# Kernel optimization log

Hardware: AMD Instinct MI355X
Metric: run time of the kernel (lower is better)

Reference implementation:

```python
import jax, jax.numpy as jnp
import numpy as np

DIM = 512; H = 8; KH = 2; G = 4; DH = 64        # dim, q heads, kv heads, GQA group, head dim
BALL = 128; SEL = 64; TOPK = 2; PDIM = 3        # sliding ball, compress/selection block, topk, pos dim
SCALE = DH ** -0.5


def _rms_norm(x, gamma):
    return x * jax.lax.rsqrt(jnp.mean(x * x, axis=-1, keepdims=True) + 1e-6) * gamma


def _rotary(t):
    # t: (B, h, S, DH); GPT-NeoX style rotate-half rotary embedding
    S = t.shape[-2]
    inv = 1.0 / (10000.0 ** (jnp.arange(0, DH, 2, dtype=jnp.float32) / DH))
    f = jnp.arange(S, dtype=jnp.float32)[:, None] * inv          # (S, DH/2)
    cos = jnp.concatenate([jnp.cos(f), jnp.cos(f)], -1)
    sin = jnp.concatenate([jnp.sin(f), jnp.sin(f)], -1)
    t1, t2 = jnp.split(t, 2, -1)
    return t * cos + jnp.concatenate([-t2, t1], -1) * sin


def _forward(x, pos, pe_w, pe_b, gamma, wq, wk, wv, k_pos, v_pos,
             k_w1, k_b1, k_w2, k_b2, v_w1, v_b1, v_w2, v_b2,
             mem_k, mem_v, w_combine, w_out, num_batches):
    B = num_batches
    # relative position of leaves wrt ball center (no-grad in original)
    p = jax.lax.stop_gradient(pos).reshape(-1, SEL, PDIM)
    rel = (p - p.mean(axis=1, keepdims=True)).reshape(-1, PDIM)
    x = x + rel @ pe_w + pe_b
    x = x.reshape(B, -1, DIM)
    S = x.shape[1]
    nb = S // SEL
    h = _rms_norm(x, gamma)
    q = (h @ wq).reshape(B, S, H, DH).transpose(0, 2, 1, 3)      # (B,H,S,DH)
    k = (h @ wk).reshape(B, S, KH, DH).transpose(0, 2, 1, 3)     # (B,KH,S,DH)
    v = (h @ wv).reshape(B, S, KH, DH).transpose(0, 2, 1, 3)
    qr, kr = _rotary(q), _rotary(k)

    # --- compressed branch: per-block intra-pos emb + MLP compression ---
    kb = k.reshape(B, KH, nb, SEL, DH) + k_pos[None, :, None]
    vb = v.reshape(B, KH, nb, SEL, DH) + v_pos[None, :, None]
    ck = jax.nn.relu(kb.reshape(B, KH, nb, SEL * DH) @ k_w1 + k_b1) @ k_w2 + k_b2
    cv = jax.nn.relu(vb.reshape(B, KH, nb, SEL * DH) @ v_w1 + v_b1) @ v_w2 + v_b2
    ck = jnp.concatenate([jnp.broadcast_to(mem_k[None], (B, KH, 1, DH)), ck], axis=2)
    cv = jnp.concatenate([jnp.broadcast_to(mem_v[None], (B, KH, 1, DH)), cv], axis=2)
    qg = qr.reshape(B, KH, G, S, DH)
    csim = jnp.einsum('bkgsd,bknd->bkgsn', qg, ck) * SCALE
    cattn = jax.nn.softmax(csim, axis=-1)
    cout = jnp.einsum('bkgsn,bknd->bkgsd', cattn, cv).reshape(B, H, S, DH)

    # --- top-k block selection from compressed attention importance ---
    imp = cattn[..., 1:].mean(axis=2)                            # share over grouped q heads: (B,KH,S,nb)
    imp_blk = imp.reshape(B, KH, nb, SEL, nb).mean(axis=3)       # per query block: (B,KH,nb,nb)
    _, sel = jax.lax.top_k(imp_blk, TOPK)                        # (B,KH,nb,TOPK)

    # --- fine branch: each query block attends own + TOPK selected blocks ---
    kblk = kr.reshape(B, KH, nb, SEL, DH)
    vblk = v.reshape(B, KH, nb, SEL, DH)
    gather = jax.vmap(jax.vmap(lambda t, s: t[s]))               # (nb,SEL,DH),(nb,TOPK)->(nb,TOPK,SEL,DH)
    fk = jnp.concatenate([gather(kblk, sel), kblk[:, :, :, None]], axis=3)
    fv = jnp.concatenate([gather(vblk, sel), vblk[:, :, :, None]], axis=3)
    fk = fk.reshape(B, KH, nb, (TOPK + 1) * SEL, DH)
    fv = fv.reshape(B, KH, nb, (TOPK + 1) * SEL, DH)
    qb = qr.reshape(B, KH, G, nb, SEL, DH)
    fsim = jnp.einsum('bkgnqd,bknmd->bkgnqm', qb, fk) * SCALE
    fout = jnp.einsum('bkgnqm,bknmd->bkgnqd', jax.nn.softmax(fsim, -1), fv)
    fout = fout.reshape(B, H, S, DH)

    # --- sliding branch: MiniBallAttn = plain SDPA within balls of size 128 ---
    nw = S // BALL
    qw = qr.reshape(B, H, nw, BALL, DH)
    kw = jnp.repeat(kr, G, axis=1).reshape(B, H, nw, BALL, DH)
    vw = jnp.repeat(v, G, axis=1).reshape(B, H, nw, BALL, DH)
    ssim = jnp.einsum('bhnqd,bhnkd->bhnqk', qw, kw) * SCALE
    sout = jnp.einsum('bhnqk,bhnkd->bhnqd', jax.nn.softmax(ssim, -1), vw)
    sout = sout.reshape(B, H, S, DH)

    # --- sigmoid-gated strategy combine, merge heads, out projection ---
    gates = jax.nn.sigmoid(h @ w_combine).reshape(B, S, H, 3).transpose(0, 2, 1, 3)
    out = gates[..., 0:1] * cout + gates[..., 1:2] * fout + gates[..., 2:3] * sout
    out = out.transpose(0, 2, 1, 3).reshape(B, S, H * DH) @ w_out
    return out.reshape(-1, DIM)


def setup_inputs() -> dict:
    key = jax.random.key(0)
    ks = jax.random.split(key, 16)
    Bn, S = 8, 4096
    N = Bn * S
    CD = SEL * DH
    def lin(k, fi, fo):
        return (jax.random.normal(k, (fi, fo), jnp.float32) / np.sqrt(fi)).astype(jnp.float32)
    return {
        'x': jax.random.normal(ks[0], (N, DIM), jnp.float32),
        'pos': jax.random.normal(ks[1], (N, PDIM), jnp.float32),
        'pe_w': lin(ks[2], PDIM, DIM),
        'pe_b': jnp.zeros((DIM,), jnp.float32),
        'gamma': jnp.ones((DIM,), jnp.float32),
        'wq': lin(ks[3], DIM, H * DH),
        'wk': lin(ks[4], DIM, KH * DH),
        'wv': lin(ks[5], DIM, KH * DH),
        'k_pos': jax.random.normal(ks[6], (KH, SEL, DH), jnp.float32) * 0.02,
        'v_pos': jax.random.normal(ks[7], (KH, SEL, DH), jnp.float32) * 0.02,
        'k_w1': lin(ks[8], CD, CD), 'k_b1': jnp.zeros((CD,), jnp.float32),
        'k_w2': lin(ks[9], CD, DH), 'k_b2': jnp.zeros((DH,), jnp.float32),
        'v_w1': lin(ks[10], CD, CD), 'v_b1': jnp.zeros((CD,), jnp.float32),
        'v_w2': lin(ks[11], CD, DH), 'v_b2': jnp.zeros((DH,), jnp.float32),
        'mem_k': jax.random.normal(ks[12], (KH, 1, DH), jnp.float32) * 0.02,
        'mem_v': jax.random.normal(ks[13], (KH, 1, DH), jnp.float32) * 0.02,
        'w_combine': lin(ks[14], DIM, 3 * H),
        'w_out': lin(ks[15], H * DH, DIM),
        'num_batches': 8,
    }


def reference(x, pos, pe_w, pe_b, gamma, wq, wk, wv, k_pos, v_pos,
              k_w1, k_b1, k_w2, k_b2, v_w1, v_b1, v_w2, v_b2,
              mem_k, mem_v, w_combine, w_out, num_batches):
    return _forward(x, pos, pe_w, pe_b, gamma, wq, wk, wv, k_pos, v_pos,
                    k_w1, k_b1, k_w2, k_b2, v_w1, v_b1, v_w2, v_b2,
                    mem_k, mem_v, w_combine, w_out, num_batches)
```

## Files before the change

kernel.cpp:

```cpp
#include <hip/hip_runtime.h>
#include <stdint.h>

#define DEVI static __device__ __forceinline__
typedef unsigned short u16;
typedef __bf16 bhalf8 __attribute__((ext_vector_type(8)));
typedef float f32x4 __attribute__((ext_vector_type(4)));

DEVI u16 f2bf(float f) {
  union { float f; unsigned u; } v; v.f = f;
  unsigned r = v.u + 0x7FFFu + ((v.u >> 16) & 1u);
  return (u16)(r >> 16);
}
DEVI float bf2f(u16 h) {
  union { unsigned u; float f; } v; v.u = ((unsigned)h) << 16;
  return v.f;
}
DEVI f32x4 MFMA(bhalf8 a, bhalf8 b, f32x4 c) {
  return __builtin_amdgcn_mfma_f32_16x16x32_bf16(a, b, c, 0, 0, 0);
}
DEVI bhalf8 LD8(const u16* p) { return *(const bhalf8*)p; }
DEVI f32x4 zero4() { f32x4 z = {0.f, 0.f, 0.f, 0.f}; return z; }

#define GLDS16(gp, lp) __builtin_amdgcn_global_load_lds( \
    (const __attribute__((address_space(1))) void*)(gp), \
// ... 196 lines not shown
      int seg = w*2 + s2;
      int r = seg*16 + sr;
      size_t ga = (size_t)(m0 + r)*K + k0 + gsc;
      size_t gb = (size_t)(n0 + r)*K + k0 + gsc;
      GLDS16(&Ah[ga], base + seg*512);
      GLDS16(&Bh[gb], base + 4096 + seg*512);
      if (SPLIT && dsp) {
        GLDS16(&Al[ga], base + 2*4096 + seg*512);
        GLDS16(&Bl[gb], base + 3*4096 + seg*512);
      }
    }
  };

  const int nt = K >> 5;
  STAGE(0, 0);
  __syncthreads();
  int cur = 0;
  for (int kt = 0; kt < nt; ++kt) {
    if (kt + 1 < nt) STAGE(cur ^ 1, (kt + 1) * 32);
    u16* bA  = sm + cur * NB * 4096;
    u16* bB  = bA + 4096;
    u16* bAl = bA + 2*4096;
    u16* bBl = bA + 3*4096;
    bhalf8 af[4], afl[4];
#pragma unroll
    for (int mf = 0; mf < 4; ++mf) {
      af[mf] = LD8(&bA[(wm*64 + mf*16 + row)*32 + kc8]);
      if (dsp) afl[mf] = LD8(&bAl[(wm*64 + mf*16 + row)*32 + kc8]);
    }
#pragma unroll
    for (int nf = 0; nf < 4; ++nf) {
      bhalf8 bfh = LD8(&bB[(wn*64 + nf*16 + row)*32 + kc8]);
      bhalf8 bfl;
      if (dsp) bfl = LD8(&bBl[(wn*64 + nf*16 + row)*32 + kc8]);
#pragma unroll
      for (int mf = 0; mf < 4; ++mf) {
        acc[mf][nf] = MFMA(af[mf], bfh, acc[mf][nf]);
        if (dsp) {
          acc[mf][nf] = MFMA(af[mf], bfl, acc[mf][nf]);
          acc[mf][nf] = MFMA(afl[mf], bfh, acc[mf][nf]);
        }
      }
    }
    __syncthreads();
    cur ^= 1;
  }
  if constexpr (EPI == 0) {
    if (n0 < 512) {
#pragma unroll
      for (int mf = 0; mf < 4; ++mf)
#pragma unroll
        for (int i = 0; i < 4; ++i) {
          int r = m0 + wm*64 + mf*16 + (l >> 4)*4 + i;
          int s = r & 4095, b = r >> 12;
#pragma unroll
          for (int nf = 0; nf < 2; ++nf) {
            int c = n0 + wn*64 + nf*16 + (l & 15);
            int hq = c >> 6, dd = c & 31;
            float t1 = acc[mf][nf][i], t2 = acc[mf][nf+2][i];
            float cs = p_cos[s*32 + dd], sn = p_sin[s*32 + dd];
            float o1 = t1*cs - t2*sn, o2 = t2*cs + t1*sn;
            size_t ob = (((size_t)(b*8 + hq))*4096 + s)*64;
            u16 h1 = f2bf(o1); out_hi[ob+dd] = h1;    out_lo[ob+dd] = f2bf(o1 - bf2f(h1));
            u16 h2 = f2bf(o2); out_hi[ob+dd+32] = h2; out_lo[ob+dd+32] = f2bf(o2 - bf2f(h2));
          }
        }
    } else if (n0 == 512) {
      int kh = wn;
#pragma unroll
      for (int mf = 0; mf < 4; ++mf)
#pragma unroll
        for (int i = 0; i < 4; ++i) {
          int r = m0 + wm*64 + mf*16 + (l >> 4)*4 + i;
          int s = r & 4095, b = r >> 12;
          int n = s >> 6, sl = s & 63;
          size_t krbase = ((size_t)(b*2 + kh)*4096 + s)*64;
          size_t kbbase = ((size_t)(b*128 + kh*64 + n))*4096 + sl*64;
#pragma unroll
          for (int nf = 0; nf < 2; ++nf) {
            int dd = nf*16 + (l & 15);
            float t1 = acc[mf][nf][i], t2 = acc[mf][nf+2][i];
            float cs = p_cos[s*32 + dd], sn = p_sin[s*32 + dd];
            krb[krbase + dd]      = f2bf(t1*cs - t2*sn);
            krb[krbase + dd + 32] = f2bf(t2*cs + t1*sn);
          }
#pragma unroll
          for (int nf = 0; nf < 4; ++nf) {
            int dk = nf*16 + (l & 15);
            float v = acc[mf][nf][i] + kpos[(kh*64 + sl)*64 + dk];
            u16 h = f2bf(v);
            kbh[kbbase + dk] = h;
            kbl[kbbase + dk] = f2bf(v - bf2f(h));
          }
        }
    } else if (n0 == 640) {
      int kh = wn;
#pragma unroll
      for (int mf = 0; mf < 4; ++mf)
#pragma unroll
        for (int i = 0; i < 4; ++i) {
          int r = m0 + wm*64 + mf*16 + (l >> 4)*4 + i;
          int s = r & 4095, b = r >> 12;
          int n = s >> 6, sl = s & 63;
          size_t v16base = ((size_t)(b*2 + kh)*4096 + s)*64;
          size_t vbbase = ((size_t)(b*128 + kh*64 + n))*4096 + sl*64;
#pragma unroll
          for (int nf = 0; nf < 4; ++nf) {
            int dv = nf*16 + (l & 15);
            float vv = acc[mf][nf][i];
            v16o[v16base + dv] = f2bf(vv);
            vbh[vbbase + dv] = f2bf(vv + vpos[(kh*64 + sl)*64 + dv]);
          }
        }
    } else {
#pragma unroll
      for (int mf = 0; mf < 4; ++mf)
#pragma unroll
        for (int nf = 0; nf < 4; ++nf)
#pragma unroll
          for (int i = 0; i < 4; ++i) {
            int r = m0 + wm*64 + mf*16 + (l >> 4)*4 + i;
            int c = n0 + wn*64 + nf*16 + (l & 15);
            if (c < 792) og[(size_t)r*24 + (c - 768)] = 1.0f / (1.0f + expf(-acc[mf][nf][i]));
          }
    }
  } else {
#pragma unroll
    for (int mf = 0; mf < 4; ++mf)
#pragma unroll
      for (int nf = 0; nf < 4; ++nf)
#pragma unroll
        for (int i = 0; i < 4; ++i) {
          int r = m0 + wm*64 + mf*16 + (l >> 4)*4 + i;
          int c = n0 + wn*64 + nf*16 + (l & 15);
          p_sin[(size_t)r*N + c] = acc[mf][nf][i];
        }
  }
}

__global__ __launch_bounds__(256) void nsa_mlp1(const u16* __restrict__ kbh, const u16* __restrict__ kbl,
    const u16* __restrict__ vbh, const u16* __restrict__ w1kh, const u16* __restrict__ w1kl,
    const u16* __restrict__ w1vh, const float* __restrict__ kb1, const float* __restrict__ vb1,
    u16* __restrict__ th, u16* __restrict__ tl, u16* __restrict__ tv) {
  __shared__ u16 sm[4 * 2 * 4096];
  const int t = threadIdx.x, w = t >> 6, l = t & 63;
  const int wm = w >> 1, wn = w & 1;
  const int bid = blockIdx.x;
  const int xcd = bid & 7, u = bid >> 3;
  const bool isK = u < 32;
  const int uu = isK ? u : u - 32;
  const int m0 = (uu & 7) * 128;
  const int n0 = (xcd * 4 + (uu >> 3)) * 128;
  const u16* Ah = isK ? kbh : vbh;
  const u16* Bh = isK ? w1kh : w1vh;
  constexpr int K = 4096;
  const int row = l & 15;
  const int kc8 = ((l >> 4) ^ ((l >> 1) & 3)) * 8;
  const int gsc = ((l & 3) ^ ((l >> 3) & 3)) * 8;
  const int sr = l >> 2;
  f32x4 acc[4][4];
#pragma unroll
  for (int a = 0; a < 4; ++a)
#pragma unroll
    for (int b = 0; b < 4; ++b) acc[a][b] = zero4();

  auto STAGE = [&](int buf, int k0) {
    u16* base = sm + buf * 4 * 4096;
#pragma unroll
    for (int s2 = 0; s2 < 2; ++s2) {
      int seg = w*2 + s2;
      int r = seg*16 + sr;
      size_t ga = (size_t)(m0 + r)*K + k0 + gsc;
      size_t gb = (size_t)(n0 + r)*K + k0 + gsc;
      GLDS16(&Ah[ga], base + seg*512);
      GLDS16(&Bh[gb], base + 4096 + seg*512);
      if (isK) {
        GLDS16(&kbl[ga], base + 2*4096 + seg*512);
        GLDS16(&w1kl[gb], base + 3*4096 + seg*512);
      }
    }
  };

  STAGE(0, 0);
  __syncthreads();
  int cur = 0;
  for (int kt = 0; kt < 128; ++kt) {
    if (kt + 1 < 128) STAGE(cur ^ 1, (kt + 1) * 32);
    u16* bA  = sm + cur * 4 * 4096;
    u16* bB  = bA + 4096;
    u16* bAl = bA + 2*4096;
    u16* bBl = bA + 3*4096;
    bhalf8 af[4], afl[4];
#pragma unroll
    for (int mf = 0; mf < 4; ++mf) {
      af[mf] = LD8(&bA[(wm*64 + mf*16 + row)*32 + kc8]);
      if (isK) afl[mf] = LD8(&bAl[(wm*64 + mf*16 + row)*32 + kc8]);
    }
#pragma unroll
    for (int nf = 0; nf < 4; ++nf) {
      bhalf8 bfh = LD8(&bB[(wn*64 + nf*16 + row)*32 + kc8]);
      bhalf8 bfl;
      if (isK) bfl = LD8(&bBl[(wn*64 + nf*16 + row)*32 + kc8]);
#pragma unroll
      for (int mf = 0; mf < 4; ++mf) {
        acc[mf][nf] = MFMA(af[mf], bfh, acc[mf][nf]);
        if (isK) {
          acc[mf][nf] = MFMA(af[mf], bfl, acc[mf][nf]);
          acc[mf][nf] = MFMA(afl[mf], bfh, acc[mf][nf]);
        }
      }
    }
    __syncthreads();
    cur ^= 1;
  }
  const float* bias = isK ? kb1 : vb1;
#pragma unroll
  for (int mf = 0; mf < 4; ++mf)
#pragma unroll
    for (int nf = 0; nf < 4; ++nf)
#pragma unroll
      for (int i = 0; i < 4; ++i) {
        int r = m0 + wm*64 + mf*16 + (l >> 4)*4 + i;
        int c = n0 + wn*64 + nf*16 + (l & 15);
        float v = fmaxf(acc[mf][nf][i] + bias[c], 0.f);
        if (isK) {
          u16 h = f2bf(v);
          th[(size_t)r*4096 + c] = h;
          tl[(size_t)r*4096 + c] = f2bf(v - bf2f(h));
        } else {
          tv[(size_t)r*4096 + c] = f2bf(v);
        }
      }
}

__global__ __launch_bounds__(256) void nsa_gemm64m(const u16* __restrict__ th, const u16* __restrict__ tl,
    const u16* __restrict__ tv, const u16* __restrict__ w2h, const u16* __restrict__ w2l,
    const u16* __restrict__ w2vh, float* __restrict__ part) {
  __shared__ u16 sm[4 * 2 * 2048];
  const int t = threadIdx.x, w = t >> 6, l = t & 63;
  const int mt = blockIdx.x;
  const bool isK = blockIdx.y < 16;
  const int kc = blockIdx.y & 15;
  const u16* Ah = isK ? th : tv;
  const u16* Bh = isK ? w2h : w2vh;
  float* po = part + (isK ? 0 : (size_t)16*1024*64);
  const int row = l & 15;
  const int kc8 = ((l >> 4) ^ ((l >> 1) & 3)) * 8;
  const int gsc = ((l & 3) ^ ((l >> 3) & 3)) * 8;
  const int sr = l >> 2;
  f32x4 acc[4];
#pragma unroll
  for (int a = 0; a < 4; ++a) acc[a] = zero4();

  auto STAGE = [&](int buf, int k0) {
    u16* base = sm + buf * 4 * 2048;
    int r = w*16 + sr;
    size_t ga = (size_t)(mt*64 + r)*4096 + k0 + gsc;
    size_t gb = (size_t)r*4096 + k0 + gsc;
    GLDS16(&Ah[ga], base + w*512);
    GLDS16(&Bh[gb], base + 2048 + w*512);
    if (isK) {
      GLDS16(&tl[ga], base + 2*2048 + w*512);
      GLDS16(&w2l[gb], base + 3*2048 + w*512);
    }
  };

  STAGE(0, kc*256);
  __syncthreads();
  int cur = 0;
  for (int kt = 0; kt < 8; ++kt) {
    if (kt + 1 < 8) STAGE(cur ^ 1, kc*256 + (kt + 1) * 32);
    u16* bA  = sm + cur * 4 * 2048;
    u16* bB  = bA + 2048;
    u16* bAl = bA + 2*2048;
    u16* bBl = bA + 3*2048;
    bhalf8 a = LD8(&bA[(w*16 + row)*32 + kc8]);
    bhalf8 al;
    if (isK) al = LD8(&bAl[(w*16 + row)*32 + kc8]);
#pragma unroll
    for (int nf = 0; nf < 4; ++nf) {
      bhalf8 b = LD8(&bB[(nf*16 + row)*32 + kc8]);
      bhalf8 bl;
      if (isK) bl = LD8(&bBl[(nf*16 + row)*32 + kc8]);
      acc[nf] = MFMA(a, b, acc[nf]);
      if (isK) {
        acc[nf] = MFMA(a, bl, acc[nf]);
        acc[nf] = MFMA(al, b, acc[nf]);
      }
    }
    __syncthreads();
    cur ^= 1;
  }
#pragma unroll
  for (int nf = 0; nf < 4; ++nf)
#pragma unroll
    for (int i = 0; i < 4; ++i) {
      int m = mt*64 + w*16 + (l >> 4)*4 + i;
      int d = nf*16 + (l & 15);
      po[((size_t)kc*1024 + m)*64 + d] = acc[nf][i];
    }
}


__global__ __launch_bounds__(256) void nsa_attn_comp(const u16* __restrict__ qrh, const u16* __restrict__ qrl,
    const u16* __restrict__ ckh, const u16* __restrict__ ckl, const u16* __restrict__ cvT,
    const float* __restrict__ g32, u16* __restrict__ comb, float* __restrict__ imp) {
  __shared__ u16 smem[24832];
  __shared__ float sImp[4 * 80];
  u16* sKh = smem;
  u16* sKl = smem + 5760;
  u16* sVT = smem + 11520;
  u16* sP  = smem + 18176;
  const int t = threadIdx.x, w = t >> 6, l = t & 63;
  const int bid = blockIdx.x;
  const int qt = bid & 63, kh = (bid >> 6) & 1, b = bid >> 7;
  const int row = l & 15, kg = (l >> 4) * 8;
  size_t kbase = (size_t)(b*2 + kh) * 80 * 64;
  size_t vbase = (size_t)(b*2 + kh) * 64 * 96;
  for (int e = t; e < 640; e += 256) {
    int r = e >> 3, c = (e & 7) * 8;
    *(int4*)&sKh[r*72 + c] = *(const int4*)&ckh[kbase + r*64 + c];
    *(int4*)&sKl[r*72 + c] = *(const int4*)&ckl[kbase + r*64 + c];
  }
  for (int e = t; e < 768; e += 256) {
    int r = e / 12, ch = e % 12;
    *(int4*)&sVT[r*104 + ch*8] = *(const int4*)&cvT[vbase + (size_t)r*96 + ch*8];
  }
  for (int e = l; e < 80; e += 64) sImp[w*80 + e] = 0.f;
#pragma unroll
  for (int i = 0; i < 4; ++i)
    sP[(w*16 + (l & 15))*104 + 80 + (l >> 4)*4 + i] = 0;
  __syncthreads();
  for (int g = 0; g < 4; ++g) {
    size_t qbase = ((size_t)((b*2 + kh)*4 + g)*4096 + qt*64) * 64 + (size_t)(w*16 + row)*64;
    bhalf8 ah0 = LD8(&qrh[qbase + kg]);
    bhalf8 ah1 = LD8(&qrh[qbase + 32 + kg]);
    bhalf8 al0 = LD8(&qrl[qbase + kg]);
    bhalf8 al1 = LD8(&qrl[qbase + 32 + kg]);
    f32x4 sc[5];
#pragma unroll
    for (int nf = 0; nf < 5; ++nf) sc[nf] = zero4();
#pragma unroll
    for (int kk = 0; kk < 2; ++kk) {
      bhalf8 ah = kk ? ah1 : ah0;
      bhalf8 al = kk ? al1 : al0;
#pragma unroll
      for (int nf = 0; nf < 5; ++nf) {
        bhalf8 bh = LD8(&sKh[(nf*16 + row)*72 + kk*32 + kg]);
        bhalf8 bl = LD8(&sKl[(nf*16 + row)*72 + kk*32 + kg]);
        sc[nf] = MFMA(ah, bh, sc[nf]);
        sc[nf] = MFMA(ah, bl, sc[nf]);
        sc[nf] = MFMA(al, bh, sc[nf]);
      }
    }
    float mx[4] = {-1e30f, -1e30f, -1e30f, -1e30f};
#pragma unroll
    for (int nf = 0; nf < 5; ++nf)
#pragma unroll
      for (int i = 0; i < 4; ++i) {
        int col = nf*16 + (l & 15);
        float v = (col < 65) ? sc[nf][i] * 0.125f : -1e30f;
        sc[nf][i] = v;
        mx[i] = fmaxf(mx[i], v);
      }
#pragma unroll
    for (int i = 0; i < 4; ++i)
#pragma unroll
      for (int o = 1; o < 16; o <<= 1) mx[i] = fmaxf(mx[i], __shfl_xor(mx[i], o));
    float sum[4] = {0.f, 0.f, 0.f, 0.f};
#pragma unroll
    for (int nf = 0; nf < 5; ++nf)
#pragma unroll
      for (int i = 0; i < 4; ++i) {
        int col = nf*16 + (l & 15);
        float p = (col < 65) ? expf(sc[nf][i] - mx[i]) : 0.f;
        sc[nf][i] = p;
        sum[i] += p;
      }
#pragma unroll
    for (int i = 0; i < 4; ++i)
#pragma unroll
      for (int o = 1; o < 16; o <<= 1) sum[i] += __shfl_xor(sum[i], o);
    float inv[4];
#pragma unroll
    for (int i = 0; i < 4; ++i) inv[i] = 1.0f / sum[i];
#pragma unroll
    for (int nf = 0; nf < 5; ++nf)
#pragma unroll
      for (int i = 0; i < 4; ++i)
        sP[(w*16 + (l >> 4)*4 + i)*104 + nf*16 + (l & 15)] = f2bf(sc[nf][i] * inv[i]);
#pragma unroll
    for (int nf = 0; nf < 5; ++nf) {
      float cs = 0.f;
#pragma unroll
      for (int i = 0; i < 4; ++i) cs += sc[nf][i] * inv[i];
      cs += __shfl_xor(cs, 16);
      cs += __shfl_xor(cs, 32);
      if (l < 16) sImp[w*80 + nf*16 + l] += cs;
    }
    f32x4 ov[4];
#pragma unroll
    for (int nf = 0; nf < 4; ++nf) ov[nf] = zero4();
#pragma unroll
    for (int kk = 0; kk < 3; ++kk) {
      bhalf8 a = LD8(&sP[(w*16 + row)*104 + kk*32 + kg]);
#pragma unroll
      for (int nf = 0; nf < 4; ++nf) {
        bhalf8 bv = LD8(&sVT[(nf*16 + row)*104 + kk*32 + kg]);
        ov[nf] = MFMA(a, bv, ov[nf]);
      }
    }
    int hq = kh*4 + g;
#pragma unroll
    for (int i = 0; i < 4; ++i) {
      int q = qt*64 + w*16 + (l >> 4)*4 + i;
      float gate = g32[((size_t)b*4096 + q)*24 + hq*3 + 0];
#pragma unroll
      for (int nf = 0; nf < 4; ++nf) {
        int d = nf*16 + (l & 15);
        comb[(((size_t)b*4096 + q)*8 + hq)*64 + d] = f2bf(gate * ov[nf][i]);
      }
    }
  }
  __syncthreads();
  if (t < 64) {
    int n = t + 1;
    imp[(size_t)bid*64 + t] = (sImp[n] + sImp[80 + n] + sImp[160 + n] + sImp[240 + n]) * (1.0f/256.0f);
  }
}

__global__ __launch_bounds__(64) void nsa_top2(const float* __restrict__ imp, int* __restrict__ sel) {
  int blk = blockIdx.x;
  int l = threadIdx.x;
  float v = imp[(size_t)blk*64 + l];
  float v1 = v; int i1 = l;
#pragma unroll
  for (int o = 1; o < 64; o <<= 1) {
    float ovv = __shfl_xor(v1, o); int oi = __shfl_xor(i1, o);
    if (ovv > v1 || (ovv == v1 && oi < i1)) { v1 = ovv; i1 = oi; }
  }
  float v2 = (l == i1) ? -3.0e38f : v; int i2 = l;
#pragma unroll
  for (int o = 1; o < 64; o <<= 1) {
    float ovv = __shfl_xor(v2, o); int oi = __shfl_xor(i2, o);
    if (ovv > v2 || (ovv == v2 && oi < i2)) { v2 = ovv; i2 = oi; }
  }
  if (l == 0) { sel[blk*2 + 0] = i1; sel[blk*2 + 1] = i2; }
}

__global__ __launch_bounds__(256) void nsa_attn_fine(const u16* __restrict__ qrh, const u16* __restrict__ kr,
    const u16* __restrict__ vT, const int* __restrict__ sel, const float* __restrict__ g32,
    u16* __restrict__ comb) {
  __shared__ u16 smem[39424];
  u16* sK  = smem;
  u16* sVT = smem + 13824;
  u16* sP  = smem + 26624;
  const int t = threadIdx.x, w = t >> 6, l = t & 63;
  const int bid = blockIdx.x;
  const int qt = bid & 63, kh = (bid >> 6) & 1, b = bid >> 7;
  const int row = l & 15, kg = (l >> 4) * 8;
  const int s0 = sel[bid*2 + 0] & 63, s1 = sel[bid*2 + 1] & 63;
  size_t kvb = (size_t)(b*2 + kh) * 4096 * 64;
  size_t vtb = (size_t)(b*2 + kh) * 64 * 4096;
  for (int e = t; e < 1536; e += 256) {
    int r = e >> 3, c = (e & 7) * 8;
    int bi = r >> 6;
    int blkid = (bi == 0) ? s0 : ((bi == 1) ? s1 : qt);
    int sidx = blkid*64 + (r & 63);
    *(int4*)&sK[r*72 + c] = *(const int4*)&kr[kvb + (size_t)sidx*64 + c];
  }
  for (int e = t; e < 1536; e += 256) {
    int r = e / 24, ch = e % 24;
    int n0 = ch * 8, bi = n0 >> 6;
    int blkid = (bi == 0) ? s0 : ((bi == 1) ? s1 : qt);
    int sidx = blkid*64 + (n0 & 63);
    *(int4*)&sVT[r*200 + n0] = *(const int4*)&vT[vtb + (size_t)r*4096 + sidx];
  }
  __syncthreads();
  for (int g = 0; g < 4; ++g) {
    size_t qbase = ((size_t)((b*2 + kh)*4 + g)*4096 + qt*64) * 64 + (size_t)(w*16 + row)*64;
    bhalf8 a0 = LD8(&qrh[qbase + kg]);
    bhalf8 a1 = LD8(&qrh[qbase + 32 + kg]);
    f32x4 sc[12];
#pragma unroll
    for (int nf = 0; nf < 12; ++nf) sc[nf] = zero4();
#pragma unroll
    for (int kk = 0; kk < 2; ++kk) {
      bhalf8 a = kk ? a1 : a0;
#pragma unroll
      for (int nf = 0; nf < 12; ++nf) {
        bhalf8 bk = LD8(&sK[(nf*16 + row)*72 + kk*32 + kg]);
        sc[nf] = MFMA(a, bk, sc[nf]);
      }
    }
    float mx[4] = {-1e30f, -1e30f, -1e30f, -1e30f};
#pragma unroll
    for (int nf = 0; nf < 12; ++nf)
#pragma unroll
      for (int i = 0; i < 4; ++i) {
        float v = sc[nf][i] * 0.125f;
        sc[nf][i] = v;
        mx[i] = fmaxf(mx[i], v);
      }
#pragma unroll
    for (int i = 0; i < 4; ++i)
#pragma unroll
      for (int o = 1; o < 16; o <<= 1) mx[i] = fmaxf(mx[i], __shfl_xor(mx[i], o));
    float sum[4] = {0.f, 0.f, 0.f, 0.f};
#pragma unroll
    for (int nf = 0; nf < 12; ++nf)
#pragma unroll
      for (int i = 0; i < 4; ++i) {
        float p = expf(sc[nf][i] - mx[i]);
        sc[nf][i] = p;
        sum[i] += p;
      }
#pragma unroll
    for (int i = 0; i < 4; ++i)
#pragma unroll
      for (int o = 1; o < 16; o <<= 1) sum[i] += __shfl_xor(sum[i], o);
    float inv[4];
#pragma unroll
    for (int i = 0; i < 4; ++i) inv[i] = 1.0f / sum[i];
#pragma unroll
    for (int nf = 0; nf < 12; ++nf)
#pragma unroll
      for (int i = 0; i < 4; ++i)
        sP[(w*16 + (l >> 4)*4 + i)*200 + nf*16 + (l & 15)] = f2bf(sc[nf][i] * inv[i]);
    f32x4 ovv[4];
#pragma unroll
    for (int nf = 0; nf < 4; ++nf) ovv[nf] = zero4();
#pragma unroll
    for (int kk = 0; kk < 6; ++kk) {
      bhalf8 a = LD8(&sP[(w*16 + row)*200 + kk*32 + kg]);
#pragma unroll
      for (int nf = 0; nf < 4; ++nf) {
        bhalf8 bv = LD8(&sVT[(nf*16 + row)*200 + kk*32 + kg]);
        ovv[nf] = MFMA(a, bv, ovv[nf]);
      }
    }
    int hq = kh*4 + g;
#pragma unroll
    for (int i = 0; i < 4; ++i) {
      int q = qt*64 + w*16 + (l >> 4)*4 + i;
      float gate = g32[((size_t)b*4096 + q)*24 + hq*3 + 1];
#pragma unroll
      for (int nf = 0; nf < 4; ++nf) {
        int d = nf*16 + (l & 15);
        size_t oi = (((size_t)b*4096 + q)*8 + hq)*64 + d;
        comb[oi] = f2bf(bf2f(comb[oi]) + gate * ovv[nf][i]);
      }
    }
  }
}

__global__ __launch_bounds__(256) void nsa_attn_slide(const u16* __restrict__ qrh, const u16* __restrict__ kr,
    const u16* __restrict__ vT, const float* __restrict__ g32, u16* __restrict__ comb) {
  __shared__ u16 smem[26624];
  u16* sK  = smem;
  u16* sVT = smem + 9216;
  u16* sP  = smem + 17920;
  const int t = threadIdx.x, w = t >> 6, l = t & 63;
  const int bid = blockIdx.x;
  const int ball = bid & 31, kh = (bid >> 5) & 1, b = bid >> 6;
  const int row = l & 15, kg = (l >> 4) * 8;
  const int ks0 = ball * 128;
  size_t kvb = (size_t)(b*2 + kh) * 4096 * 64;
  size_t vtb = (size_t)(b*2 + kh) * 64 * 4096;
  for (int e = t; e < 1024; e += 256) {
    int r = e >> 3, c = (e & 7) * 8;
    *(int4*)&sK[r*72 + c] = *(const int4*)&kr[kvb + (size_t)(ks0 + r)*64 + c];
  }
  for (int e = t; e < 1024; e += 256) {
    int r = e >> 4, ch = e & 15;
    *(int4*)&sVT[r*136 + ch*8] = *(const int4*)&vT[vtb + (size_t)r*4096 + ks0 + ch*8];
  }
  __syncthreads();
  for (int hq = 0; hq < 4; ++hq) {
    int hh = kh*4 + hq;
    for (int qh = 0; qh < 2; ++qh) {
      int qt = ball*2 + qh;
      size_t qbase = ((size_t)(b*8 + hh)*4096 + qt*64) * 64 + (size_t)(w*16 + row)*64;
      bhalf8 a0 = LD8(&qrh[qbase + kg]);
      bhalf8 a1 = LD8(&qrh[qbase + 32 + kg]);
      f32x4 sc[8];
#pragma unroll
      for (int nf = 0; nf < 8; ++nf) sc[nf] = zero4();
#pragma unroll
      for (int kk = 0; kk < 2; ++kk) {
        bhalf8 a = kk ? a1 : a0;
#pragma unroll
        for (int nf = 0; nf < 8; ++nf) {
          bhalf8 bk = LD8(&sK[(nf*16 + row)*72 + kk*32 + kg]);
          sc[nf] = MFMA(a, bk, sc[nf]);
        }
      }
      float mx[4] = {-1e30f, -1e30f, -1e30f, -1e30f};
#pragma unroll
      for (int nf = 0; nf < 8; ++nf)
#pragma unroll
        for (int i = 0; i < 4; ++i) {
          float v = sc[nf][i] * 0.125f;
          sc[nf][i] = v;
          mx[i] = fmaxf(mx[i], v);
        }
#pragma unroll
      for (int i = 0; i < 4; ++i)
#pragma unroll
        for (int o = 1; o < 16; o <<= 1) mx[i] = fmaxf(mx[i], __shfl_xor(mx[i], o));
      float sum[4] = {0.f, 0.f, 0.f, 0.f};
#pragma unroll
      for (int nf = 0; nf < 8; ++nf)
#pragma unroll
        for (int i = 0; i < 4; ++i) {
          float p = expf(sc[nf][i] - mx[i]);
          sc[nf][i] = p;
          sum[i] += p;
        }
#pragma unroll
      for (int i = 0; i < 4; ++i)
#pragma unroll
        for (int o = 1; o < 16; o <<= 1) sum[i] += __shfl_xor(sum[i], o);
      float inv[4];
#pragma unroll
      for (int i = 0; i < 4; ++i) inv[i] = 1.0f / sum[i];
#pragma unroll
      for (int nf = 0; nf < 8; ++nf)
#pragma unroll
        for (int i = 0; i < 4; ++i)
          sP[(w*16 + (l >> 4)*4 + i)*136 + nf*16 + (l & 15)] = f2bf(sc[nf][i] * inv[i]);
      f32x4 ovv[4];
#pragma unroll
      for (int nf = 0; nf < 4; ++nf) ovv[nf] = zero4();
#pragma unroll
      for (int kk = 0; kk < 4; ++kk) {
        bhalf8 a = LD8(&sP[(w*16 + row)*136 + kk*32 + kg]);
#pragma unroll
        for (int nf = 0; nf < 4; ++nf) {
          bhalf8 bv = LD8(&sVT[(nf*16 + row)*136 + kk*32 + kg]);
          ovv[nf] = MFMA(a, bv, ovv[nf]);
        }
      }
#pragma unroll
      for (int i = 0; i < 4; ++i) {
        int q = qt*64 + w*16 + (l >> 4)*4 + i;
        float gate = g32[((size_t)b*4096 + q)*24 + hh*3 + 2];
#pragma unroll
        for (int nf = 0; nf < 4; ++nf) {
          int d = nf*16 + (l & 15);
          size_t oi = (((size_t)b*4096 + q)*8 + hh)*64 + d;
          comb[oi] = f2bf(bf2f(comb[oi]) + gate * ovv[nf][i]);
        }
      }
    }
  }
}


extern "C" void kernel_launch(void* const* d_in, const int* in_sizes, int n_in,
                              void* d_out, int out_size, void* d_ws, size_t ws_size,
                              hipStream_t stream) {
  const float* x     = (const float*)d_in[0];
  const float* pos   = (const float*)d_in[1];
  const float* pe_w  = (const float*)d_in[2];
  const float* pe_b  = (const float*)d_in[3];
  const float* gamma = (const float*)d_in[4];
  const float* wq    = (const float*)d_in[5];
  const float* wk    = (const float*)d_in[6];
  const float* wv    = (const float*)d_in[7];
  const float* k_pos = (const float*)d_in[8];
  const float* v_pos = (const float*)d_in[9];
  const float* k_w1  = (const float*)d_in[10];
  const float* k_b1  = (const float*)d_in[11];
  const float* k_w2  = (const float*)d_in[12];
  const float* k_b2  = (const float*)d_in[13];
  const float* v_w1  = (const float*)d_in[14];
  const float* v_b1  = (const float*)d_in[15];
  const float* v_w2  = (const float*)d_in[16];
  const float* v_b2  = (const float*)d_in[17];
  const float* mem_k = (const float*)d_in[18];
  const float* mem_v = (const float*)d_in[19];
  const float* w_cmb = (const float*)d_in[20];
  const float* w_out = (const float*)d_in[21];
  float* out = (float*)d_out;
  char* ws = (char*)d_ws;

  size_t off = 0;
  auto A = [&](size_t b) { size_t o = off; off += (b + 255) & ~(size_t)255; return o; };
  const size_t oR1 = A(100663296);
  const size_t oR2 = A(67108864);
  const size_t oR4 = A(16777216);
  const size_t oR5 = A(16777216);
  const size_t oR6 = A(16777216);
  const size_t oR7 = A(16777216);
  const size_t oR8 = A(3145728);
  const size_t oR9 = A(2097152);
  const size_t o_cos = A(524288),  o_sin = A(524288);
  const size_t o_ckh = A(163840),  o_ckl = A(163840);
  const size_t o_cvT = A(196608);
  const size_t o_woh = A(524288);
  const size_t o_imp = A(262144);
  const size_t o_sel = A(8192);
  const size_t o_part = A(8388608);

  if (ws_size < off) {
    nsa_sentinel<<<(out_size + 255)/256, 256, 0, stream>>>(out, out_size, (float)(ws_size >> 20));
    return;
  }

#define WP(T, o) ((T*)(ws + (o)))
  u16*  h_hi = WP(u16, oR1);           u16* h_lo = WP(u16, oR1 + 33554432);
  u16*  w1kh = WP(u16, oR1);           u16* w1kl = WP(u16, oR1 + 33554432);
  u16*  w1vh = WP(u16, oR1 + 67108864);
  u16*  combp = WP(u16, oR1);
  u16*  qrh  = WP(u16, oR2);           u16* qrl  = WP(u16, oR2 + 33554432);
  u16*  th   = WP(u16, oR4);           u16* tl   = WP(u16, oR4 + 8388608);
  u16*  v16b = WP(u16, oR5);           u16* vbh  = WP(u16, oR5 + 8388608);
  u16*  tv   = WP(u16, oR5);
  u16*  kbh  = WP(u16, oR6);           u16* kbl  = WP(u16, oR6 + 8388608);
  u16*  krb  = WP(u16, oR7);           u16* vTb  = WP(u16, oR7 + 8388608);
  float* g32 = WP(float, oR8);
  u16*  wch  = WP(u16, oR9);           u16* wcl  = WP(u16, oR9 + 917504);
  u16*  w2h  = WP(u16, oR9);           u16* w2l  = WP(u16, oR9 + 524288);
  u16*  w2vh = WP(u16, oR9 + 1048576);
  float* cosb = WP(float, o_cos);      float* sinb = WP(float, o_sin);
  u16*  ckh  = WP(u16, o_ckh);         u16* ckl  = WP(u16, o_ckl);
  u16*  cvT  = WP(u16, o_cvT);
  u16*  woh  = WP(u16, o_woh);
  float* imp = WP(float, o_imp);
  int*  selp = WP(int, o_sel);
  float* part = WP(float, o_part);

  nsa_hnorm<<<32768, 256, 0, stream>>>(x, pos, pe_w, pe_b, gamma, h_hi, h_lo);
  nsa_wcat_rope<<<2304, 256, 0, stream>>>(wq, wk, wv, w_cmb, wch, wcl, cosb, sinb);
  nsa_gemm<true, 0><<<dim3(256, 7, 1), 256, 0, stream>>>(h_hi, h_lo, wch, wcl, 512, 896,
      cosb, sinb, qrh, qrl, g32, k_pos, v_pos, krb, kbh, kbl, v16b, vbh);
  nsa_vT16<<<1024, 256, 0, stream>>>(v16b, vTb);
  nsa_wT2<<<dim3(64, 64, 2), 256, 0, stream>>>(k_w1, w1kh, w1kl, v_w1, w1vh, nullptr, 4096, 4096);
  nsa_wT2<<<dim3(64, 1, 2), 256, 0, stream>>>(k_w2, w2h, w2l, v_w2, w2vh, nullptr, 4096, 64);
  nsa_mlp1<<<512, 256, 0, stream>>>(kbh, kbl, vbh, w1kh, w1kl, w1vh, k_b1, v_b1, th, tl, tv);
  nsa_gemm64m<<<dim3(16, 32), 256, 0, stream>>>(th, tl, tv, w2h, w2l, w2vh, part);
  nsa_red_ckcv<<<704, 256, 0, stream>>>(part, mem_k, k_b2, mem_v, v_b2, ckh, ckl, cvT);
  nsa_attn_comp<<<1024, 256, 0, stream>>>(qrh, qrl, ckh, ckl, cvT, g32, combp, imp);
  nsa_top2<<<1024, 64, 0, stream>>>(imp, selp);
  nsa_attn_fine<<<1024, 256, 0, stream>>>(qrh, krb, vTb, selp, g32, combp);
  nsa_attn_slide<<<512, 256, 0, stream>>>(qrh, krb, vTb, g32, combp);
  nsa_wT<<<dim3(8, 8), 256, 0, stream>>>(w_out, woh, nullptr, 512, 512);
  nsa_gemm<false, 2><<<dim3(256, 4, 1), 256, 0, stream>>>(combp, nullptr, woh, nullptr, 512, 512,
      nullptr, out, nullptr, nullptr, nullptr, nullptr, nullptr, nullptr, nullptr, nullptr,
      nullptr, nullptr);
#undef WP
}
```

Before: 694.1 us.

## Merge sliding-window attention into compressed attention launch with separate output buffer

The sliding-window attention blocks now run inside the compressed-attention kernel as an extra 512 blocks, writing to a separate buffer. The fine-selection kernel adds that buffer into the combined output, so the separate slide launch and its read-modify-write of the combined tensor go away. This lets the independent sliding and compressed work share one grid and removes a launch, at the cost of an extra 32 MB buffer read in the fine kernel and more divergent code per kernel.

```diff
diff --git a/kernel.cpp b/kernel.cpp
--- a/kernel.cpp
+++ b/kernel.cpp
@@ -522,130 +522,229 @@
 }
 
 
-__global__ __launch_bounds__(256) void nsa_attn_comp(const u16* __restrict__ qrh, const u16* __restrict__ qrl,
+__global__ __launch_bounds__(256) void nsa_attn_cs(const u16* __restrict__ qrh, const u16* __restrict__ qrl,
     const u16* __restrict__ ckh, const u16* __restrict__ ckl, const u16* __restrict__ cvT,
-    const float* __restrict__ g32, u16* __restrict__ comb, float* __restrict__ imp) {
-  __shared__ u16 smem[24832];
+    const u16* __restrict__ kr, const u16* __restrict__ vT, const float* __restrict__ g32,
+    u16* __restrict__ comb_c, u16* __restrict__ comb_s, float* __restrict__ imp) {
+  __shared__ u16 smem[26624];
   __shared__ float sImp[4 * 80];
-  u16* sKh = smem;
-  u16* sKl = smem + 5760;
-  u16* sVT = smem + 11520;
-  u16* sP  = smem + 18176;
   const int t = threadIdx.x, w = t >> 6, l = t & 63;
-  const int bid = blockIdx.x;
-  const int qt = bid & 63, kh = (bid >> 6) & 1, b = bid >> 7;
   const int row = l & 15, kg = (l >> 4) * 8;
-  size_t kbase = (size_t)(b*2 + kh) * 80 * 64;
-  size_t vbase = (size_t)(b*2 + kh) * 64 * 96;
-  for (int e = t; e < 640; e += 256) {
-    int r = e >> 3, c = (e & 7) * 8;
-    *(int4*)&sKh[r*72 + c] = *(const int4*)&ckh[kbase + r*64 + c];
-    *(int4*)&sKl[r*72 + c] = *(const int4*)&ckl[kbase + r*64 + c];
-  }
-  for (int e = t; e < 768; e += 256) {
-    int r = e / 12, ch = e % 12;
-    *(int4*)&sVT[r*104 + ch*8] = *(const int4*)&cvT[vbase + (size_t)r*96 + ch*8];
-  }
-  for (int e = l; e < 80; e += 64) sImp[w*80 + e] = 0.f;
-#pragma unroll
-  for (int i = 0; i < 4; ++i)
-    sP[(w*16 + (l & 15))*104 + 80 + (l >> 4)*4 + i] = 0;
-  __syncthreads();
-  for (int g = 0; g < 4; ++g) {
-    size_t qbase = ((size_t)((b*2 + kh)*4 + g)*4096 + qt*64) * 64 + (size_t)(w*16 + row)*64;
-    bhalf8 ah0 = LD8(&qrh[qbase + kg]);
-    bhalf8 ah1 = LD8(&qrh[qbase + 32 + kg]);
-    bhalf8 al0 = LD8(&qrl[qbase + kg]);
-    bhalf8 al1 = LD8(&qrl[qbase + 32 + kg]);
-    f32x4 sc[5];
-#pragma unroll
-    for (int nf = 0; nf < 5; ++nf) sc[nf] = zero4();
-#pragma unroll
-    for (int kk = 0; kk < 2; ++kk) {
-      bhalf8 ah = kk ? ah1 : ah0;
-      bhalf8 al = kk ? al1 : al0;
+  if (blockIdx.x < 512) {
+    u16* sK  = smem;
+    u16* sVT = smem + 9216;
+    u16* sP  = smem + 17920;
+    const int bid = blockIdx.x;
+    const int ball = bid & 31, kh = (bid >> 5) & 1, b = bid >> 6;
+    const int ks0 = ball * 128;
+    size_t kvb = (size_t)(b*2 + kh) * 4096 * 64;
+    size_t vtb = (size_t)(b*2 + kh) * 64 * 4096;
+    for (int e = t; e < 1024; e += 256) {
+      int r = e >> 3, c = (e & 7) * 8;
+      *(int4*)&sK[r*72 + c] = *(const int4*)&kr[kvb + (size_t)(ks0 + r)*64 + c];
+    }
+    for (int e = t; e < 1024; e += 256) {
+      int r = e >> 4, ch = e & 15;
+      *(int4*)&sVT[r*136 + ch*8] = *(const int4*)&vT[vtb + (size_t)r*4096 + ks0 + ch*8];
+    }
+    __syncthreads();
+    for (int hq = 0; hq < 4; ++hq) {
+      int hh = kh*4 + hq;
+      for (int qh = 0; qh < 2; ++qh) {
+        int qt = ball*2 + qh;
+        size_t qbase = ((size_t)(b*8 + hh)*4096 + qt*64) * 64 + (size_t)(w*16 + row)*64;
+        bhalf8 a0 = LD8(&qrh[qbase + kg]);
+        bhalf8 a1 = LD8(&qrh[qbase + 32 + kg]);
+        f32x4 sc[8];
+#pragma unroll
+        for (int nf = 0; nf < 8; ++nf) sc[nf] = zero4();
+#pragma unroll
+        for (int kk = 0; kk < 2; ++kk) {
+          bhalf8 a = kk ? a1 : a0;
+#pragma unroll
+          for (int nf = 0; nf < 8; ++nf) {
+            bhalf8 bk = LD8(&sK[(nf*16 + row)*72 + kk*32 + kg]);
+            sc[nf] = MFMA(a, bk, sc[nf]);
+          }
+        }
+        float mx[4] = {-1e30f, -1e30f, -1e30f, -1e30f};
+#pragma unroll
+        for (int nf = 0; nf < 8; ++nf)
+#pragma unroll
+          for (int i = 0; i < 4; ++i) {
+            float v = sc[nf][i] * 0.125f;
+            sc[nf][i] = v;
+            mx[i] = fmaxf(mx[i], v);
+          }
+#pragma unroll
+        for (int i = 0; i < 4; ++i)
+#pragma unroll
+          for (int o = 1; o < 16; o <<= 1) mx[i] = fmaxf(mx[i], __shfl_xor(mx[i], o));
+        float sum[4] = {0.f, 0.f, 0.f, 0.f};
+#pragma unroll
+        for (int nf = 0; nf < 8; ++nf)
+#pragma unroll
+          for (int i = 0; i < 4; ++i) {
+            float p = expf(sc[nf][i] - mx[i]);
+            sc[nf][i] = p;
+            sum[i] += p;
+          }
+#pragma unroll
+        for (int i = 0; i < 4; ++i)
+#pragma unroll
+          for (int o = 1; o < 16; o <<= 1) sum[i] += __shfl_xor(sum[i], o);
+        float inv[4];
+#pragma unroll
+        for (int i = 0; i < 4; ++i) inv[i] = 1.0f / sum[i];
+#pragma unroll
+        for (int nf = 0; nf < 8; ++nf)
+#pragma unroll
+          for (int i = 0; i < 4; ++i)
+            sP[(w*16 + (l >> 4)*4 + i)*136 + nf*16 + (l & 15)] = f2bf(sc[nf][i] * inv[i]);
+        f32x4 ovv[4];
+#pragma unroll
+        for (int nf = 0; nf < 4; ++nf) ovv[nf] = zero4();
+#pragma unroll
+        for (int kk = 0; kk < 4; ++kk) {
+          bhalf8 a = LD8(&sP[(w*16 + row)*136 + kk*32 + kg]);
+#pragma unroll
+          for (int nf = 0; nf < 4; ++nf) {
+            bhalf8 bv = LD8(&sVT[(nf*16 + row)*136 + kk*32 + kg]);
+            ovv[nf] = MFMA(a, bv, ovv[nf]);
+          }
+        }
+#pragma unroll
+        for (int i = 0; i < 4; ++i) {
+          int q = qt*64 + w*16 + (l >> 4)*4 + i;
+          float gate = g32[((size_t)b*4096 + q)*24 + hh*3 + 2];
+#pragma unroll
+          for (int nf = 0; nf < 4; ++nf) {
+            int d = nf*16 + (l & 15);
+            size_t oi = (((size_t)b*4096 + q)*8 + hh)*64 + d;
+            comb_s[oi] = f2bf(gate * ovv[nf][i]);
+          }
+        }
+      }
+    }
+  } else {
+    u16* sKh = smem;
+    u16* sKl = smem + 5760;
+    u16* sVT = smem + 11520;
+    u16* sP  = smem + 18176;
+    const int bid = blockIdx.x - 512;
+    const int qt = bid & 63, kh = (bid >> 6) & 1, b = bid >> 7;
+    size_t kbase = (size_t)(b*2 + kh) * 80 * 64;
+    size_t vbase = (size_t)(b*2 + kh) * 64 * 96;
+    for (int e = t; e < 640; e += 256) {
+      int r = e >> 3, c = (e & 7) * 8;
+      *(int4*)&sKh[r*72 + c] = *(const int4*)&ckh[kbase + r*64 + c];
+      *(int4*)&sKl[r*72 + c] = *(const int4*)&ckl[kbase + r*64 + c];
+    }
+    for (int e = t; e < 768; e += 256) {
+      int r = e / 12, ch = e % 12;
+      *(int4*)&sVT[r*104 + ch*8] = *(const int4*)&cvT[vbase + (size_t)r*96 + ch*8];
+    }
+    for (int e = l; e < 80; e += 64) sImp[w*80 + e] = 0.f;
+#pragma unroll
+    for (int i = 0; i < 4; ++i)
+      sP[(w*16 + (l & 15))*104 + 80 + (l >> 4)*4 + i] = 0;
+    __syncthreads();
+    for (int g = 0; g < 4; ++g) {
+      size_t qbase = ((size_t)((b*2 + kh)*4 + g)*4096 + qt*64) * 64 + (size_t)(w*16 + row)*64;
+      bhalf8 ah0 = LD8(&qrh[qbase + kg]);
+      bhalf8 ah1 = LD8(&qrh[qbase + 32 + kg]);
+      bhalf8 al0 = LD8(&qrl[qbase + kg]);
+      bhalf8 al1 = LD8(&qrl[qbase + 32 + kg]);
+      f32x4 sc[5];
+#pragma unroll
+      for (int nf = 0; nf < 5; ++nf) sc[nf] = zero4();
+#pragma unroll
+      for (int kk = 0; kk < 2; ++kk) {
+        bhalf8 ah = kk ? ah1 : ah0;
+        bhalf8 al = kk ? al1 : al0;
+#pragma unroll
+        for (int nf = 0; nf < 5; ++nf) {
+          bhalf8 bh = LD8(&sKh[(nf*16 + row)*72 + kk*32 + kg]);
+          bhalf8 bl = LD8(&sKl[(nf*16 + row)*72 + kk*32 + kg]);
+          sc[nf] = MFMA(ah, bh, sc[nf]);
+          sc[nf] = MFMA(ah, bl, sc[nf]);
+          sc[nf] = MFMA(al, bh, sc[nf]);
+        }
+      }
+      float mx[4] = {-1e30f, -1e30f, -1e30f, -1e30f};
+#pragma unroll
+      for (int nf = 0; nf < 5; ++nf)
+#pragma unroll
+        for (int i = 0; i < 4; ++i) {
+          int col = nf*16 + (l & 15);
+          float v = (col < 65) ? sc[nf][i] * 0.125f : -1e30f;
+          sc[nf][i] = v;
+          mx[i] = fmaxf(mx[i], v);
+        }
+#pragma unroll
+      for (int i = 0; i < 4; ++i)
+#pragma unroll
+        for (int o = 1; o < 16; o <<= 1) mx[i] = fmaxf(mx[i], __shfl_xor(mx[i], o));
+      float sum[4] = {0.f, 0.f, 0.f, 0.f};
+#pragma unroll
+      for (int nf = 0; nf < 5; ++nf)
+#pragma unroll
+        for (int i = 0; i < 4; ++i) {
+          int col = nf*16 + (l & 15);
+          float p = (col < 65) ? expf(sc[nf][i] - mx[i]) : 0.f;
+          sc[nf][i] = p;
+          sum[i] += p;
+        }
+#pragma unroll
+      for (int i = 0; i < 4; ++i)
+#pragma unroll
+        for (int o = 1; o < 16; o <<= 1) sum[i] += __shfl_xor(sum[i], o);
+      float inv[4];
+#pragma unroll
+      for (int i = 0; i < 4; ++i) inv[i] = 1.0f / sum[i];
+#pragma unroll
+      for (int nf = 0; nf < 5; ++nf)
+#pragma unroll
+        for (int i = 0; i < 4; ++i)
+          sP[(w*16 + (l >> 4)*4 + i)*104 + nf*16 + (l & 15)] = f2bf(sc[nf][i] * inv[i]);
 #pragma unroll
       for (int nf = 0; nf < 5; ++nf) {
-        bhalf8 bh = LD8(&sKh[(nf*16 + row)*72 + kk*32 + kg]);
-        bhalf8 bl = LD8(&sKl[(nf*16 + row)*72 + kk*32 + kg]);
-        sc[nf] = MFMA(ah, bh, sc[nf]);
-        sc[nf] = MFMA(ah, bl, sc[nf]);
-        sc[nf] = MFMA(al, bh, sc[nf]);
-      }
-    }
-    float mx[4] = {-1e30f, -1e30f, -1e30f, -1e30f};
-#pragma unroll
-    for (int nf = 0; nf < 5; ++nf)
+        float cs = 0.f;
+#pragma unroll
+        for (int i = 0; i < 4; ++i) cs += sc[nf][i] * inv[i];
+        cs += __shfl_xor(cs, 16);
+        cs += __shfl_xor(cs, 32);
+        if (l < 16) sImp[w*80 + nf*16 + l] += cs;
+      }
+      f32x4 ov[4];
+#pragma unroll
+      for (int nf = 0; nf < 4; ++nf) ov[nf] = zero4();
+#pragma unroll
+      for (int kk = 0; kk < 3; ++kk) {
+        bhalf8 a = LD8(&sP[(w*16 + row)*104 + kk*32 + kg]);
+#pragma unroll
+        for (int nf = 0; nf < 4; ++nf) {
+          bhalf8 bv = LD8(&sVT[(nf*16 + row)*104 + kk*32 + kg]);
+          ov[nf] = MFMA(a, bv, ov[nf]);
+        }
+      }
+      int hq = kh*4 + g;
 #pragma unroll
       for (int i = 0; i < 4; ++i) {
-        int col = nf*16 + (l & 15);
-        float v = (col < 65) ? sc[nf][i] * 0.125f : -1e30f;
-        sc[nf][i] = v;
-        mx[i] = fmaxf(mx[i], v);
-      }
-#pragma unroll
-    for (int i = 0; i < 4; ++i)
-#pragma unroll
-      for (int o = 1; o < 16; o <<= 1) mx[i] = fmaxf(mx[i], __shfl_xor(mx[i], o));
-    float sum[4] = {0.f, 0.f, 0.f, 0.f};
-#pragma unroll
-    for (int nf = 0; nf < 5; ++nf)
-#pragma unroll
-      for (int i = 0; i < 4; ++i) {
-        int col = nf*16 + (l & 15);
-        float p = (col < 65) ? expf(sc[nf][i] - mx[i]) : 0.f;
-        sc[nf][i] = p;
-        sum[i] += p;
-      }
-#pragma unroll
-    for (int i = 0; i < 4; ++i)
-#pragma unroll
-      for (int o = 1; o < 16; o <<= 1) sum[i] += __shfl_xor(sum[i], o);
-    float inv[4];
-#pragma unroll
-    for (int i = 0; i < 4; ++i) inv[i] = 1.0f / sum[i];
-#pragma unroll
-    for (int nf = 0; nf < 5; ++nf)
-#pragma unroll
-      for (int i = 0; i < 4; ++i)
-        sP[(w*16 + (l >> 4)*4 + i)*104 + nf*16 + (l & 15)] = f2bf(sc[nf][i] * inv[i]);
-#pragma unroll
-    for (int nf = 0; nf < 5; ++nf) {
-      float cs = 0.f;
-#pragma unroll
-      for (int i = 0; i < 4; ++i) cs += sc[nf][i] * inv[i];
-      cs += __shfl_xor(cs, 16);
-      cs += __shfl_xor(cs, 32);
-      if (l < 16) sImp[w*80 + nf*16 + l] += cs;
-    }
-    f32x4 ov[4];
-#pragma unroll
-    for (int nf = 0; nf < 4; ++nf) ov[nf] = zero4();
-#pragma unroll
-    for (int kk = 0; kk < 3; ++kk) {
-      bhalf8 a = LD8(&sP[(w*16 + row)*104 + kk*32 + kg]);
-#pragma unroll
-      for (int nf = 0; nf < 4; ++nf) {
-        bhalf8 bv = LD8(&sVT[(nf*16 + row)*104 + kk*32 + kg]);
-        ov[nf] = MFMA(a, bv, ov[nf]);
-      }
-    }
-    int hq = kh*4 + g;
-#pragma unroll
-    for (int i = 0; i < 4; ++i) {
-      int q = qt*64 + w*16 + (l >> 4)*4 + i;
-      float gate = g32[((size_t)b*4096 + q)*24 + hq*3 + 0];
-#pragma unroll
-      for (int nf = 0; nf < 4; ++nf) {
-        int d = nf*16 + (l & 15);
-        comb[(((size_t)b*4096 + q)*8 + hq)*64 + d] = f2bf(gate * ov[nf][i]);
-      }
-    }
-  }
-  __syncthreads();
-  if (t < 64) {
-    int n = t + 1;
-    imp[(size_t)bid*64 + t] = (sImp[n] + sImp[80 + n] + sImp[160 + n] + sImp[240 + n]) * (1.0f/256.0f);
+        int q = qt*64 + w*16 + (l >> 4)*4 + i;
+        float gate = g32[((size_t)b*4096 + q)*24 + hq*3 + 0];
+#pragma unroll
+        for (int nf = 0; nf < 4; ++nf) {
+          int d = nf*16 + (l & 15);
+          comb_c[(((size_t)b*4096 + q)*8 + hq)*64 + d] = f2bf(gate * ov[nf][i]);
+        }
+      }
+    }
+    __syncthreads();
+    if (t < 64) {
+      int n = t + 1;
+      imp[(size_t)bid*64 + t] = (sImp[n] + sImp[80 + n] + sImp[160 + n] + sImp[240 + n]) * (1.0f/256.0f);
+    }
   }
 }
 
@@ -670,7 +769,7 @@
 
 __global__ __launch_bounds__(256) void nsa_attn_fine(const u16* __restrict__ qrh, const u16* __restrict__ kr,
     const u16* __restrict__ vT, const int* __restrict__ sel, const float* __restrict__ g32,
-    u16* __restrict__ comb) {
+    u16* __restrict__ comb_c, const u16* __restrict__ comb_s) {
   __shared__ u16 smem[39424];
   u16* sK  = smem;
   u16* sVT = smem + 13824;
@@ -768,109 +867,7 @@
       for (int nf = 0; nf < 4; ++nf) {
         int d = nf*16 + (l & 15);
         size_t oi = (((size_t)b*4096 + q)*8 + hq)*64 + d;
-        comb[oi] = f2bf(bf2f(comb[oi]) + gate * ovv[nf][i]);
-      }
-    }
-  }
-}
-
-__global__ __launch_bounds__(256) void nsa_attn_slide(const u16* __restrict__ qrh, const u16* __restrict__ kr,
-    const u16* __restrict__ vT, const float* __restrict__ g32, u16* __restrict__ comb) {
-  __shared__ u16 smem[26624];
-  u16* sK  = smem;
-  u16* sVT = smem + 9216;
-  u16* sP  = smem + 17920;
-  const int t = threadIdx.x, w = t >> 6, l = t & 63;
-  const int bid = blockIdx.x;
-  const int ball = bid & 31, kh = (bid >> 5) & 1, b = bid >> 6;
-  const int row = l & 15, kg = (l >> 4) * 8;
-  const int ks0 = ball * 128;
-  size_t kvb = (size_t)(b*2 + kh) * 4096 * 64;
-  size_t vtb = (size_t)(b*2 + kh) * 64 * 4096;
-  for (int e = t; e < 1024; e += 256) {
-    int r = e >> 3, c = (e & 7) * 8;
-    *(int4*)&sK[r*72 + c] = *(const int4*)&kr[kvb + (size_t)(ks0 + r)*64 + c];
-  }
-  for (int e = t; e < 1024; e += 256) {
-    int r = e >> 4, ch = e & 15;
-    *(int4*)&sVT[r*136 + ch*8] = *(const int4*)&vT[vtb + (size_t)r*4096 + ks0 + ch*8];
-  }
-  __syncthreads();
-  for (int hq = 0; hq < 4; ++hq) {
-    int hh = kh*4 + hq;
-    for (int qh = 0; qh < 2; ++qh) {
-      int qt = ball*2 + qh;
-      size_t qbase = ((size_t)(b*8 + hh)*4096 + qt*64) * 64 + (size_t)(w*16 + row)*64;
-      bhalf8 a0 = LD8(&qrh[qbase + kg]);
-      bhalf8 a1 = LD8(&qrh[qbase + 32 + kg]);
-      f32x4 sc[8];
-#pragma unroll
-      for (int nf = 0; nf < 8; ++nf) sc[nf] = zero4();
-#pragma unroll
-      for (int kk = 0; kk < 2; ++kk) {
-        bhalf8 a = kk ? a1 : a0;
-#pragma unroll
-        for (int nf = 0; nf < 8; ++nf) {
-          bhalf8 bk = LD8(&sK[(nf*16 + row)*72 + kk*32 + kg]);
-          sc[nf] = MFMA(a, bk, sc[nf]);
-        }
-      }
-      float mx[4] = {-1e30f, -1e30f, -1e30f, -1e30f};
-#pragma unroll
-      for (int nf = 0; nf < 8; ++nf)
-#pragma unroll
-        for (int i = 0; i < 4; ++i) {
-          float v = sc[nf][i] * 0.125f;
-          sc[nf][i] = v;
-          mx[i] = fmaxf(mx[i], v);
-        }
-#pragma unroll
-      for (int i = 0; i < 4; ++i)
-#pragma unroll
-        for (int o = 1; o < 16; o <<= 1) mx[i] = fmaxf(mx[i], __shfl_xor(mx[i], o));
-      float sum[4] = {0.f, 0.f, 0.f, 0.f};
-#pragma unroll
-      for (int nf = 0; nf < 8; ++nf)
-#pragma unroll
-        for (int i = 0; i < 4; ++i) {
-          float p = expf(sc[nf][i] - mx[i]);
-          sc[nf][i] = p;
-          sum[i] += p;
-        }
-#pragma unroll
-      for (int i = 0; i < 4; ++i)
-#pragma unroll
-        for (int o = 1; o < 16; o <<= 1) sum[i] += __shfl_xor(sum[i], o);
-      float inv[4];
-#pragma unroll
-      for (int i = 0; i < 4; ++i) inv[i] = 1.0f / sum[i];
-#pragma unroll
-      for (int nf = 0; nf < 8; ++nf)
-#pragma unroll
-        for (int i = 0; i < 4; ++i)
-          sP[(w*16 + (l >> 4)*4 + i)*136 + nf*16 + (l & 15)] = f2bf(sc[nf][i] * inv[i]);
-      f32x4 ovv[4];
-#pragma unroll
-      for (int nf = 0; nf < 4; ++nf) ovv[nf] = zero4();
-#pragma unroll
-      for (int kk = 0; kk < 4; ++kk) {
-        bhalf8 a = LD8(&sP[(w*16 + row)*136 + kk*32 + kg]);
-#pragma unroll
-        for (int nf = 0; nf < 4; ++nf) {
-          bhalf8 bv = LD8(&sVT[(nf*16 + row)*136 + kk*32 + kg]);
-          ovv[nf] = MFMA(a, bv, ovv[nf]);
-        }
-      }
-#pragma unroll
-      for (int i = 0; i < 4; ++i) {
-        int q = qt*64 + w*16 + (l >> 4)*4 + i;
-        float gate = g32[((size_t)b*4096 + q)*24 + hh*3 + 2];
-#pragma unroll
-        for (int nf = 0; nf < 4; ++nf) {
-          int d = nf*16 + (l & 15);
-          size_t oi = (((size_t)b*4096 + q)*8 + hh)*64 + d;
-          comb[oi] = f2bf(bf2f(comb[oi]) + gate * ovv[nf][i]);
-        }
+        comb_c[oi] = f2bf(bf2f(comb_c[oi]) + bf2f(comb_s[oi]) + gate * ovv[nf][i]);
       }
     }
   }
@@ -932,7 +929,8 @@
   u16*  h_hi = WP(u16, oR1);           u16* h_lo = WP(u16, oR1 + 33554432);
   u16*  w1kh = WP(u16, oR1);           u16* w1kl = WP(u16, oR1 + 33554432);
   u16*  w1vh = WP(u16, oR1 + 67108864);
-  u16*  combp = WP(u16, oR1);
+  u16*  combc = WP(u16, oR1);
+  u16*  combs = WP(u16, oR1 + 33554432);
   u16*  qrh  = WP(u16, oR2);           u16* qrl  = WP(u16, oR2 + 33554432);
   u16*  th   = WP(u16, oR4);           u16* tl   = WP(u16, oR4 + 8388608);
   u16*  v16b = WP(u16, oR5);           u16* vbh  = WP(u16, oR5 + 8388608);
@@ -961,12 +959,11 @@
   nsa_mlp1<<<512, 256, 0, stream>>>(kbh, kbl, vbh, w1kh, w1kl, w1vh, k_b1, v_b1, th, tl, tv);
   nsa_gemm64m<<<dim3(16, 32), 256, 0, stream>>>(th, tl, tv, w2h, w2l, w2vh, part);
   nsa_red_ckcv<<<704, 256, 0, stream>>>(part, mem_k, k_b2, mem_v, v_b2, ckh, ckl, cvT);
-  nsa_attn_comp<<<1024, 256, 0, stream>>>(qrh, qrl, ckh, ckl, cvT, g32, combp, imp);
+  nsa_attn_cs<<<1536, 256, 0, stream>>>(qrh, qrl, ckh, ckl, cvT, krb, vTb, g32, combc, combs, imp);
   nsa_top2<<<1024, 64, 0, stream>>>(imp, selp);
-  nsa_attn_fine<<<1024, 256, 0, stream>>>(qrh, krb, vTb, selp, g32, combp);
-  nsa_attn_slide<<<512, 256, 0, stream>>>(qrh, krb, vTb, g32, combp);
+  nsa_attn_fine<<<1024, 256, 0, stream>>>(qrh, krb, vTb, selp, g32, combc, combs);
   nsa_wT<<<dim3(8, 8), 256, 0, stream>>>(w_out, woh, nullptr, 512, 512);
-  nsa_gemm<false, 2><<<dim3(256, 4, 1), 256, 0, stream>>>(combp, nullptr, woh, nullptr, 512, 512,
+  nsa_gemm<false, 2><<<dim3(256, 4, 1), 256, 0, stream>>>(combc, nullptr, woh, nullptr, 512, 512,
       nullptr, out, nullptr, nullptr, nullptr, nullptr, nullptr, nullptr, nullptr, nullptr,
       nullptr, nullptr);
 #undef WP
```

Result: no change. 687.3 us (-1.0%).
